# Kernel tuning notes

Measured on AMD Instinct MI355X. Metric: run time of the kernel, lower is better.

Reference implementation:

```python
import jax, jax.numpy as jnp
import numpy as np

TAU = 0.5
EPS = 1e-12  # F.normalize default eps


def _projection(z, fc1_w, fc1_b, fc2_w, fc2_b):
    h = jax.nn.elu(z @ fc1_w.T + fc1_b)
    return h @ fc2_w.T + fc2_b


def _normalize(z):
    n = jnp.linalg.norm(z, axis=1, keepdims=True)
    return z / jnp.maximum(n, EPS)


def _semi_loss(h1, h2):
    z1 = _normalize(h1)
    z2 = _normalize(h2)
    refl_sim = jnp.exp((z1 @ z1.T) / TAU)      # [N, N]
    between_sim = jnp.exp((z1 @ z2.T) / TAU)   # [N, N]
    pos = jnp.diagonal(between_sim)
    denom = refl_sim.sum(axis=1) + between_sim.sum(axis=1) - jnp.diagonal(refl_sim)
    return -jnp.log(pos / denom)


def setup_inputs() -> dict:
    key = jax.random.key(0)
    k1, k2, k3, k4 = jax.random.split(key, 4)
    N, H, P = 8192, 512, 512
    s1 = 1.0 / np.sqrt(H)
    s2 = 1.0 / np.sqrt(P)
    return {
        "z1": jax.random.normal(k1, (N, H), jnp.float32),
        "z2": jax.random.normal(k2, (N, H), jnp.float32),
        "fc1_w": jax.random.normal(k3, (P, H), jnp.float32) * s1,
        "fc1_b": jnp.zeros((P,), jnp.float32),
        "fc2_w": jax.random.normal(k4, (H, P), jnp.float32) * s2,
        "fc2_b": jnp.zeros((H,), jnp.float32),
    }


def reference(z1, z2, fc1_w, fc1_b, fc2_w, fc2_b):
    h1 = _projection(z1, fc1_w, fc1_b, fc2_w, fc2_b)
    h2 = _projection(z2, fc1_w, fc1_b, fc2_w, fc2_b)
    l1 = _semi_loss(h1, h2)
    l2 = _semi_loss(h2, h1)
    ret = (l1 + l2) * 0.5
    return ret.mean()
```

## Files before the change

kernel.cpp:

```cpp
#include <hip/hip_runtime.h>
#include <math.h>

typedef __attribute__((ext_vector_type(8))) __bf16 bf16x8;
typedef __attribute__((ext_vector_type(4))) float f32x4;
typedef __attribute__((ext_vector_type(16))) float f32x16;
typedef __attribute__((ext_vector_type(8))) unsigned short u16x8;
typedef __attribute__((ext_vector_type(8))) int i32x8;

#define GAS(p) ((const __attribute__((address_space(1))) void*)(p))
#define LAS(p) ((__attribute__((address_space(3))) void*)(p))

__device__ __forceinline__ unsigned short f2bf(float f) {
  union { float f; unsigned int u; } v; v.f = f;
  unsigned int r = (v.u + 0x7FFFu + ((v.u >> 16) & 1u)) >> 16;
  return (unsigned short)r;
}
__device__ __forceinline__ float bf2f(unsigned short b) {
  union { unsigned int u; float f; } v; v.u = ((unsigned int)b) << 16;
  return v.f;
}

__global__ __launch_bounds__(256) void cast_all_kernel(
    const float* __restrict__ z1, const float* __restrict__ z2,
    const float* __restrict__ w1, const float* __restrict__ w2,
    unsigned short* __restrict__ z1b, unsigned short* __restrict__ z2b,
    unsigned short* __restrict__ w1b, unsigned short* __restrict__ w2b) {
  int b = blockIdx.x;
  if (b < 8192) {
    const float* in = (b < 4096) ? z1 : z2;
    unsigned short* out = (b < 4096) ? z1b : z2b;
    int base = (b < 4096) ? b : b - 4096;
    int i = (base * 256 + threadIdx.x) * 4;
    float4 v = *(const float4*)(in + i);
    ushort4 o;
    o.x = f2bf(v.x); o.y = f2bf(v.y); o.z = f2bf(v.z); o.w = f2bf(v.w);
    *(ushort4*)(out + i) = o;
  } else {
    const float* in = (b < 8448) ? w1 : w2;
    unsigned short* out = (b < 8448) ? w1b : w2b;
    int base = (b < 8448) ? b - 8192 : b - 8448;
    int i = (base * 256 + threadIdx.x) * 4;
    float4 v = *(const float4*)(in + i);
    unsigned int lo = (unsigned)f2bf(v.x) | ((unsigned)f2bf(v.y) << 16);
    unsigned int hi = (unsigned)f2bf(v.z) | ((unsigned)f2bf(v.w) << 16);
    const int col = i >> 9, k = i & 511;
    const size_t dst = (size_t)(col >> 5) * 32768 + (size_t)(k >> 4) * 1024
                     + (size_t)((k >> 3) & 1) * 512 + (col & 31) * 16 + (k & 7) * 2;
    *(int2*)((char*)out + dst) = make_int2((int)lo, (int)hi);
  }
}

template<int EPI>
__global__ __launch_bounds__(256, 4)
void proj_kernel(const unsigned short* __restrict__ A1,
                 const unsigned short* __restrict__ A2,
                 const unsigned short* __restrict__ Wf,
                 const float* __restrict__ bias,
                 unsigned short* __restrict__ C1,
                 unsigned short* __restrict__ C2) {
  __shared__ unsigned short lA[2][4096];
  const int b = blockIdx.x;
  const int which = b >> 9;
  const int r = b & 511;
  const int m0 = (r >> 3) * 64;
  const int n0 = (r & 7) * 64;
  const unsigned short* A = which ? A2 : A1;
  unsigned short* C = which ? C2 : C1;

  const int tid  = threadIdx.x;
  const int wv   = tid >> 6;
  const int lane = tid & 63;
  const int half = lane >> 5;
  const int l31  = lane & 31;

  const int srow0 = wv * 8 + (lane >> 3);
  const int srow1 = srow0 + 32;
  const int sc0 = ((lane & 7) * 16) ^ ((srow0 & 7) << 4);
  const int sc1 = ((lane & 7) * 16) ^ ((srow1 & 7) << 4);
  const int sdst0 = wv * 1024 + lane * 16;
  const int sdst1 = sdst0 + 4096;
  const char* Ac = (const char*)A;

#define PROJ_STAGE(buf, kc)                                                    \
  do {                                                                         \
    const size_t kb = (size_t)(kc) * 128;                                      \
    __builtin_amdgcn_global_load_lds(                                          \
        GAS(Ac + (size_t)(m0 + srow0) * 1024 + kb + sc0),                      \
        LAS((char*)&lA[buf][0] + sdst0), 16, 0, 0);                            \
    __builtin_amdgcn_global_load_lds(                                          \
        GAS(Ac + (size_t)(m0 + srow1) * 1024 + kb + sc1),                      \
        LAS((char*)&lA[buf][0] + sdst1), 16, 0, 0);                            \
  } while (0)

  const int arow = (wv & 1) * 32 + l31;
  const int aoff = arow * 128;
  const int aswz = (arow & 7) << 4;
  const char* Wb = (const char*)Wf
                 + (size_t)((n0 >> 5) + (wv >> 1)) * 32768
                 + half * 512 + l31 * 16;

  f32x16 acc;
#pragma unroll
  for (int i = 0; i < 16; ++i) acc[i] = 0.f;

  PROJ_STAGE(0, 0);
  __syncthreads();

  for (int kc = 0; kc < 8; ++kc) {
    if (kc < 7) PROJ_STAGE((kc + 1) & 1, kc + 1);
    const char* bufA = (const char*)&lA[kc & 1][0];
#pragma unroll
    for (int s = 0; s < 4; ++s) {
      bf16x8 av = *(const bf16x8*)(bufA + aoff + ((s * 32 + half * 16) ^ aswz));
      bf16x8 bv = *(const bf16x8*)(Wb + (size_t)(kc * 4 + s) * 1024);
      acc = __builtin_amdgcn_mfma_f32_32x32x16_bf16(av, bv, acc, 0, 0, 0);
    }
    __syncthreads();
  }
#undef PROJ_STAGE

  const int col = n0 + (wv >> 1) * 32 + l31;
  const float bvs = bias[col];
#pragma unroll
  for (int reg = 0; reg < 16; ++reg) {
    const int row = m0 + (wv & 1) * 32 + (reg & 3) + 8 * (reg >> 2) + 4 * half;
    float v = acc[reg] + bvs;
    if constexpr (EPI == 0) v = (v > 0.f) ? v : expm1f(v);
    C[(size_t)row * 512 + col] = f2bf(v);
  }
}

__global__ __launch_bounds__(256, 2)
void gram_kernel(const unsigned char* __restrict__ q1,
                 const unsigned char* __restrict__ q2,
                 float* __restrict__ d11, float* __restrict__ d22,
                 float* __restrict__ d12r, float* __restrict__ d12c) {
  __shared__ unsigned char lA[65536];

  const int b = blockIdx.x;
  const unsigned char *Abase, *Bbase;
  float *rptr, *cptr;
  int by, g, cnt;
  bool cross;
  if (b < 1088) {
    const bool first = (b < 544);
    int j = first ? b : b - 544;
    int q = (int)((sqrtf(2.f * j + 1.f) - 1.f) * 0.5f);
    while (2 * (q + 1) * (q + 2) <= j) ++q;
    while (2 * q * (q + 1) > j) --q;
    const int w = j - 2 * q * (q + 1);
    const int dr = w / (q + 1);
    g = w - dr * (q + 1);
    by = 4 * q + dr;
    const unsigned char* h = first ? q1 : q2;
    Abase = h; Bbase = h;
    rptr = first ? d11 : d22; cptr = rptr;
    cnt = min(4, by + 1 - g * 4);
    cross = false;
  } else {
    const int j = b - 1088;
    g = j >> 6; by = j & 63;
    Abase = q1; Bbase = q2;
    rptr = d12r; cptr = d12c;
    cnt = 4; cross = true;
  }

  const int tid  = threadIdx.x;
  const int wave = tid >> 6;
  const int lane = tid & 63;
  const int half = lane >> 5;
  const int l31  = lane & 31;
  const int pa0 = (wave & 1) * 2;
  const int pb0 = (wave >> 1) * 2;
  const int lfo = half * 1024 + l31 * 16;

  {
    const unsigned char* Asrc = Abase + (size_t)(by * 4 + wave) * 16384 + lane * 16;
    unsigned char* Adst = lA + wave * 16384 + lane * 16;
#pragma unroll
    for (int i = 0; i < 16; ++i)
      __builtin_amdgcn_global_load_lds(GAS(Asrc + i * 1024),
                                       LAS(Adst + i * 1024), 16, 0, 0);
  }
  __syncthreads();

  union frag { i32x8 v; int4 h[2]; };

  float rs[2][16];
#pragma unroll
  for (int mi = 0; mi < 2; ++mi)
#pragma unroll
    for (int rr = 0; rr < 16; ++rr) rs[mi][rr] = 0.f;

  for (int t = 0; t < cnt; ++t) {
    const int ct = g * 4 + t;
    const unsigned char* B0 = Bbase + (size_t)(ct * 4 + pb0) * 16384 + lfo;
    const unsigned char* B1 = B0 + 16384;

    f32x16 acc[2][2];
#pragma unroll
    for (int i = 0; i < 2; ++i)
#pragma unroll
      for (int jj = 0; jj < 2; ++jj)
#pragma unroll
        for (int rr = 0; rr < 16; ++rr) acc[i][jj][rr] = 0.f;

#pragma unroll
    for (int KT = 0; KT < 4; ++KT) {
#pragma unroll
      for (int ktl = 0; ktl < 2; ++ktl) {
        const int ko = KT * 4096 + ktl * 2048;
        frag fa[2], fb[2];
        fb[0].h[0] = *(const int4*)(B0 + ko);
        fb[0].h[1] = *(const int4*)(B0 + ko + 512);
        fb[1].h[0] = *(const int4*)(B1 + ko);
        fb[1].h[1] = *(const int4*)(B1 + ko + 512);
#pragma unroll
        for (int i = 0; i < 2; ++i) {
          const int oa = (pa0 + i) * 16384 + ko + lfo;
          fa[i].h[0] = *(const int4*)&lA[oa];
          fa[i].h[1] = *(const int4*)&lA[oa + 512];
        }
#pragma unroll
        for (int mi = 0; mi < 2; ++mi)
#pragma unroll
          for (int ni = 0; ni < 2; ++ni)
            acc[mi][ni] = __builtin_amdgcn_mfma_scale_f32_32x32x64_f8f6f4(
                fa[mi].v, fb[ni].v, acc[mi][ni],
                0, 0,
                0, 0x7F7F7F7F,
                0, 0x7F7F7F7F);
      }
    }

    float cs[2] = {0.f, 0.f};
#pragma unroll
    for (int mi = 0; mi < 2; ++mi)
#pragma unroll
      for (int ni = 0; ni < 2; ++ni)
#pragma unroll
        for (int rr = 0; rr < 16; ++rr) {
          float v = exp2f(2.8853900817779268f * acc[mi][ni][rr]);
          rs[mi][rr] += v;
          cs[ni] += v;
        }
    const bool diag = (!cross) && (ct == by);
    if (!diag) {
#pragma unroll
      for (int ni = 0; ni < 2; ++ni) {
        float v = cs[ni] + __shfl_xor(cs[ni], 32, 64);
        if (half == 0)
          atomicAdd(&cptr[ct * 128 + (wave >> 1) * 64 + ni * 32 + l31], v);
      }
    }
  }

#pragma unroll
  for (int mi = 0; mi < 2; ++mi) {
#pragma unroll
    for (int dd = 1; dd < 32; dd <<= 1) {
#pragma unroll
      for (int rr = 0; rr < 16; ++rr) rs[mi][rr] += __shfl_xor(rs[mi][rr], dd, 64);
    }
    if (l31 == 0) {
      const int mb = by * 128 + (wave & 1) * 64 + mi * 32;
#pragma unroll
      for (int rr = 0; rr < 16; ++rr) {
        const int row = mb + (rr & 3) + 8 * (rr >> 2) + 4 * half;
        atomicAdd(&rptr[row], rs[mi][rr]);
      }
    }
  }
}

__global__ __launch_bounds__(256)
void norm_diag_kernel(const unsigned short* __restrict__ h1,
                      const unsigned short* __restrict__ h2,
                      unsigned char* __restrict__ q1,
                      unsigned char* __restrict__ q2,
                      float* __restrict__ cdiag) {
  const int wave = threadIdx.x >> 6, lane = threadIdx.x & 63;
  const int row = blockIdx.x * 4 + wave;
  const u16x8 u1 = *(const u16x8*)(h1 + (size_t)row * 512 + lane * 8);
  const u16x8 u2 = *(const u16x8*)(h2 + (size_t)row * 512 + lane * 8);
  float f1[8], f2[8], ss1 = 0.f, ss2 = 0.f;
#pragma unroll
  for (int j = 0; j < 8; ++j) {
    f1[j] = bf2f(u1[j]); ss1 += f1[j] * f1[j];
    f2[j] = bf2f(u2[j]); ss2 += f2[j] * f2[j];
  }
#pragma unroll
  for (int d = 1; d < 64; d <<= 1) {
    ss1 += __shfl_xor(ss1, d, 64);
    ss2 += __shfl_xor(ss2, d, 64);
  }
  const float inv1 = 1.0f / fmaxf(sqrtf(ss1), 1e-12f);
  const float inv2 = 1.0f / fmaxf(sqrtf(ss2), 1e-12f);
  float a[8], bb[8];
  float dot = 0.f;
#pragma unroll
  for (int j = 0; j < 8; ++j) {
    a[j] = f1[j] * inv1; bb[j] = f2[j] * inv2;
    dot += a[j] * bb[j];
  }
  int lo1 = __builtin_amdgcn_cvt_pk_fp8_f32(a[0], a[1], 0, false);
  lo1 = __builtin_amdgcn_cvt_pk_fp8_f32(a[2], a[3], lo1, true);
  int hi1 = __builtin_amdgcn_cvt_pk_fp8_f32(a[4], a[5], 0, false);
  hi1 = __builtin_amdgcn_cvt_pk_fp8_f32(a[6], a[7], hi1, true);
  int lo2 = __builtin_amdgcn_cvt_pk_fp8_f32(bb[0], bb[1], 0, false);
  lo2 = __builtin_amdgcn_cvt_pk_fp8_f32(bb[2], bb[3], lo2, true);
  int hi2 = __builtin_amdgcn_cvt_pk_fp8_f32(bb[4], bb[5], 0, false);
  hi2 = __builtin_amdgcn_cvt_pk_fp8_f32(bb[6], bb[7], hi2, true);

  const int c0 = lane * 8;
  const size_t dst = (size_t)(row >> 5) * 16384 + (c0 >> 6) * 2048
                   + ((c0 >> 4) & 3) * 512 + (row & 31) * 16 + (c0 & 15);
  *(int2*)(q1 + dst) = make_int2(lo1, hi1);
  *(int2*)(q2 + dst) = make_int2(lo2, hi2);
#pragma unroll
  for (int d = 1; d < 64; d <<= 1) dot += __shfl_xor(dot, d, 64);
  if (lane == 0) cdiag[row] = dot;
}

__global__ __launch_bounds__(256)
void finalize_kernel(const float* __restrict__ d11, const float* __restrict__ d22,
                     const float* __restrict__ d12r, const float* __restrict__ d12c,
                     const float* __restrict__ cdiag, float* __restrict__ out) {
  const float e2 = 7.38905609893065f;
  float s = 0.f;
  for (int i = threadIdx.x; i < 8192; i += 256) {
    const float den1 = d11[i] + d12r[i] - e2;
    const float den2 = d22[i] + d12c[i] - e2;
    s += -2.0f * cdiag[i] + 0.5f * (logf(den1) + logf(den2));
  }
#pragma unroll
  for (int d = 1; d < 64; d <<= 1) s += __shfl_xor(s, d, 64);
  __shared__ float sm[4];
  if ((threadIdx.x & 63) == 0) sm[threadIdx.x >> 6] = s;
  __syncthreads();
  if (threadIdx.x == 0) out[0] = (sm[0] + sm[1] + sm[2] + sm[3]) * (1.0f / 8192.0f);
}

extern "C" void kernel_launch(void* const* d_in, const int* in_sizes, int n_in,
                              void* d_out, int out_size, void* d_ws, size_t ws_size,
                              hipStream_t stream) {
  const float* z1 = (const float*)d_in[0];
  const float* z2 = (const float*)d_in[1];
  const float* w1 = (const float*)d_in[2];
  const float* b1 = (const float*)d_in[3];
  const float* w2 = (const float*)d_in[4];
  const float* b2 = (const float*)d_in[5];
  float* out = (float*)d_out;

  const int N = 8192, D = 512;
  char* ws = (char*)d_ws;
  auto alloc = [&](size_t bytes) {
    char* p = ws; ws += (bytes + 255) & ~(size_t)255; return p;
  };
  unsigned short* z1b = (unsigned short*)alloc((size_t)N * D * 2);
  unsigned short* z2b = (unsigned short*)alloc((size_t)N * D * 2);
  unsigned short* g1  = (unsigned short*)alloc((size_t)N * D * 2);
  unsigned short* g2  = (unsigned short*)alloc((size_t)N * D * 2);
  unsigned short* w1b = (unsigned short*)alloc((size_t)D * D * 2);
  unsigned short* w2b = (unsigned short*)alloc((size_t)D * D * 2);
  float* sums  = (float*)alloc((size_t)4 * N * sizeof(float));
  float* cdiag = (float*)alloc((size_t)N * sizeof(float));
  float* d11 = sums, *d22 = sums + N, *d12r = sums + 2 * N, *d12c = sums + 3 * N;
  unsigned short* h1 = z1b;
  unsigned short* h2 = z2b;
  unsigned char* q1 = (unsigned char*)g1;
  unsigned char* q2 = (unsigned char*)g2;

  hipMemsetAsync(sums, 0, (size_t)4 * N * sizeof(float), stream);

  cast_all_kernel<<<dim3(8704), 256, 0, stream>>>(z1, z2, w1, w2, z1b, z2b, w1b, w2b);
  proj_kernel<0><<<dim3(1024), 256, 0, stream>>>(z1b, z2b, w1b, b1, g1, g2);
  proj_kernel<1><<<dim3(1024), 256, 0, stream>>>(g1, g2, w2b, b2, h1, h2);
  norm_diag_kernel<<<dim3(N / 4), 256, 0, stream>>>(h1, h2, q1, q2, cdiag);
  gram_kernel<<<dim3(2112), 256, 0, stream>>>(q1, q2, d11, d22, d12r, d12c);
  finalize_kernel<<<1, 256, 0, stream>>>(d11, d22, d12r, d12c, cdiag, out);
}
```

Measured before the change: 244.7 us.

## Split gram tile across eight waves with one A panel per wave

The gram kernel now launches 512 threads per block, and each of eight waves computes a 32x64 sub-tile instead of four waves each computing 64x64. Each wave keeps half the accumulators and row sums, which lowers register pressure and raises the occupancy target to 4 blocks. The A-tile copy into shared memory is spread across all 512 threads. In exchange, each B fragment is now loaded from global memory by four waves instead of two, doubling B traffic per MFMA, and the LDS use of 64KB per block may cap how many blocks fit per CU.

```diff
diff --git a/kernel.cpp b/kernel.cpp
--- a/kernel.cpp
+++ b/kernel.cpp
@@ -130,7 +130,7 @@
   }
 }
 
-__global__ __launch_bounds__(256, 2)
+__global__ __launch_bounds__(512, 4)
 void gram_kernel(const unsigned char* __restrict__ q1,
                  const unsigned char* __restrict__ q2,
                  float* __restrict__ d11, float* __restrict__ d22,
@@ -166,109 +166,97 @@
   }
 
   const int tid  = threadIdx.x;
-  const int wave = tid >> 6;
+  const int wv   = tid >> 6;
   const int lane = tid & 63;
   const int half = lane >> 5;
   const int l31  = lane & 31;
-  const int pa0 = (wave & 1) * 2;
-  const int pb0 = (wave >> 1) * 2;
-  const int lfo = half * 1024 + l31 * 16;
+  const int rw   = wv & 3;
+  const int cw   = wv >> 2;
+  const int lfo  = half * 1024 + l31 * 16;
 
   {
-    const unsigned char* Asrc = Abase + (size_t)(by * 4 + wave) * 16384 + lane * 16;
-    unsigned char* Adst = lA + wave * 16384 + lane * 16;
-#pragma unroll
-    for (int i = 0; i < 16; ++i)
-      __builtin_amdgcn_global_load_lds(GAS(Asrc + i * 1024),
-                                       LAS(Adst + i * 1024), 16, 0, 0);
+    const unsigned char* Asrc = Abase + (size_t)by * 65536 + tid * 16;
+    unsigned char* Adst = lA + tid * 16;
+#pragma unroll
+    for (int i = 0; i < 8; ++i)
+      __builtin_amdgcn_global_load_lds(GAS(Asrc + i * 8192),
+                                       LAS(Adst + i * 8192), 16, 0, 0);
   }
   __syncthreads();
 
   union frag { i32x8 v; int4 h[2]; };
 
-  float rs[2][16];
-#pragma unroll
-  for (int mi = 0; mi < 2; ++mi)
-#pragma unroll
-    for (int rr = 0; rr < 16; ++rr) rs[mi][rr] = 0.f;
+  float rs[16];
+#pragma unroll
+  for (int rr = 0; rr < 16; ++rr) rs[rr] = 0.f;
+
+  const unsigned char* Apan = lA + rw * 16384 + lfo;
+  const unsigned char* baseB = Bbase + (size_t)(2 * cw) * 16384 + lfo;
 
   for (int t = 0; t < cnt; ++t) {
     const int ct = g * 4 + t;
-    const unsigned char* B0 = Bbase + (size_t)(ct * 4 + pb0) * 16384 + lfo;
+    const unsigned char* B0 = baseB + (size_t)ct * 65536;
     const unsigned char* B1 = B0 + 16384;
 
-    f32x16 acc[2][2];
-#pragma unroll
-    for (int i = 0; i < 2; ++i)
-#pragma unroll
-      for (int jj = 0; jj < 2; ++jj)
-#pragma unroll
-        for (int rr = 0; rr < 16; ++rr) acc[i][jj][rr] = 0.f;
+    f32x16 acc[2];
+#pragma unroll
+    for (int ni = 0; ni < 2; ++ni)
+#pragma unroll
+      for (int rr = 0; rr < 16; ++rr) acc[ni][rr] = 0.f;
 
 #pragma unroll
     for (int KT = 0; KT < 4; ++KT) {
 #pragma unroll
       for (int ktl = 0; ktl < 2; ++ktl) {
         const int ko = KT * 4096 + ktl * 2048;
-        frag fa[2], fb[2];
+        frag fa, fb[2];
         fb[0].h[0] = *(const int4*)(B0 + ko);
         fb[0].h[1] = *(const int4*)(B0 + ko + 512);
         fb[1].h[0] = *(const int4*)(B1 + ko);
         fb[1].h[1] = *(const int4*)(B1 + ko + 512);
-#pragma unroll
-        for (int i = 0; i < 2; ++i) {
-          const int oa = (pa0 + i) * 16384 + ko + lfo;
-          fa[i].h[0] = *(const int4*)&lA[oa];
-          fa[i].h[1] = *(const int4*)&lA[oa + 512];
-        }
-#pragma unroll
-        for (int mi = 0; mi < 2; ++mi)
-#pragma unroll
-          for (int ni = 0; ni < 2; ++ni)
-            acc[mi][ni] = __builtin_amdgcn_mfma_scale_f32_32x32x64_f8f6f4(
-                fa[mi].v, fb[ni].v, acc[mi][ni],
-                0, 0,
-                0, 0x7F7F7F7F,
-                0, 0x7F7F7F7F);
+        fa.h[0] = *(const int4*)(Apan + ko);
+        fa.h[1] = *(const int4*)(Apan + ko + 512);
+#pragma unroll
+        for (int ni = 0; ni < 2; ++ni)
+          acc[ni] = __builtin_amdgcn_mfma_scale_f32_32x32x64_f8f6f4(
+              fa.v, fb[ni].v, acc[ni],
+              0, 0,
+              0, 0x7F7F7F7F,
+              0, 0x7F7F7F7F);
       }
     }
 
     float cs[2] = {0.f, 0.f};
 #pragma unroll
-    for (int mi = 0; mi < 2; ++mi)
-#pragma unroll
-      for (int ni = 0; ni < 2; ++ni)
-#pragma unroll
-        for (int rr = 0; rr < 16; ++rr) {
-          float v = exp2f(2.8853900817779268f * acc[mi][ni][rr]);
-          rs[mi][rr] += v;
-          cs[ni] += v;
-        }
+    for (int ni = 0; ni < 2; ++ni)
+#pragma unroll
+      for (int rr = 0; rr < 16; ++rr) {
+        float v = exp2f(2.8853900817779268f * acc[ni][rr]);
+        rs[rr] += v;
+        cs[ni] += v;
+      }
     const bool diag = (!cross) && (ct == by);
     if (!diag) {
 #pragma unroll
       for (int ni = 0; ni < 2; ++ni) {
         float v = cs[ni] + __shfl_xor(cs[ni], 32, 64);
         if (half == 0)
-          atomicAdd(&cptr[ct * 128 + (wave >> 1) * 64 + ni * 32 + l31], v);
+          atomicAdd(&cptr[ct * 128 + cw * 64 + ni * 32 + l31], v);
       }
     }
   }
 
 #pragma unroll
-  for (int mi = 0; mi < 2; ++mi) {
-#pragma unroll
-    for (int dd = 1; dd < 32; dd <<= 1) {
-#pragma unroll
-      for (int rr = 0; rr < 16; ++rr) rs[mi][rr] += __shfl_xor(rs[mi][rr], dd, 64);
-    }
-    if (l31 == 0) {
-      const int mb = by * 128 + (wave & 1) * 64 + mi * 32;
-#pragma unroll
-      for (int rr = 0; rr < 16; ++rr) {
-        const int row = mb + (rr & 3) + 8 * (rr >> 2) + 4 * half;
-        atomicAdd(&rptr[row], rs[mi][rr]);
-      }
+  for (int dd = 1; dd < 32; dd <<= 1) {
+#pragma unroll
+    for (int rr = 0; rr < 16; ++rr) rs[rr] += __shfl_xor(rs[rr], dd, 64);
+  }
+  if (l31 == 0) {
+    const int mb = by * 128 + rw * 32;
+#pragma unroll
+    for (int rr = 0; rr < 16; ++rr) {
+      const int row = mb + (rr & 3) + 8 * (rr >> 2) + 4 * half;
+      atomicAdd(&rptr[row], rs[rr]);
     }
   }
 }
@@ -377,6 +365,6 @@
   proj_kernel<0><<<dim3(1024), 256, 0, stream>>>(z1b, z2b, w1b, b1, g1, g2);
   proj_kernel<1><<<dim3(1024), 256, 0, stream>>>(g1, g2, w2b, b2, h1, h2);
   norm_diag_kernel<<<dim3(N / 4), 256, 0, stream>>>(h1, h2, q1, q2, cdiag);
-  gram_kernel<<<dim3(2112), 256, 0, stream>>>(q1, q2, d11, d22, d12r, d12c);
+  gram_kernel<<<dim3(2112), 512, 0, stream>>>(q1, q2, d11, d22, d12r, d12c);
   finalize_kernel<<<1, 256, 0, stream>>>(d11, d22, d12r, d12c, cdiag, out);
 }
```

Result: slower. 462.0 us (+88.8%).
